# Kernel optimization log

Hardware: AMD Instinct MI355X
Metric: run time of the kernel (lower is better)

Reference implementation:

```python
import jax, jax.numpy as jnp
import numpy as np
import math

N_NODES = 4096
DEG = 32
N_EDGES = N_NODES * DEG
H = 128
NUM_NODE_STATES = 4
NUM_EDGE_STATES = 4
NUM_GRAPHS = 64
UPPER_T, LOWER_T, NUM_ITERS, TEMP_EVAL = 1.0, 0.1, 10000, 0.1
TRAINING_STEP = 1000
NEG_INF = -1.0e9


def temp_by_step(step):
    # linear anneal upper->lower over NUM_ITERS; eval temp when step == -1
    if step == -1:
        return TEMP_EVAL
    frac = min(step / float(NUM_ITERS), 1.0)
    return UPPER_T + (LOWER_T - UPPER_T) * frac


def from_binary_states(bits):
    w = 2 ** jnp.arange(bits.shape[-1], dtype=jnp.int32)
    return jnp.sum(bits.astype(jnp.int32) * w, axis=-1)


def group_argmax_onehot(vals, group, num_segments):
    # gumbel_softmax(vals, group, tau=0, use_noise=False): one-hot argmax per group
    seg_max = jax.ops.segment_max(vals, group, num_segments=num_segments)
    return (vals >= seg_max[group]).astype(jnp.int32)


def layernorm(x, g, b, eps=1e-5):
    mu = jnp.mean(x, -1, keepdims=True)
    var = jnp.mean((x - mu) ** 2, -1, keepdims=True)
    return (x - mu) * jax.lax.rsqrt(var + eps) * g + b


def select_best(emb, bits, scalars, index, num_index):
    states = 2 * from_binary_states(bits)                  # even state codes
    group = states * num_index + index.astype(jnp.int32)   # unique (state, index) id
    best = group_argmax_onehot(-scalars[:, 0], group, emb.shape[0] * num_index)
    return emb[states + best]


def _forward(node_states, edge_states, scalars, edge_index, batch_vec,
             reverse_idx, edge_pos, training_step,
             emb_virtual, emb_reciever, emb_edge, emb_static,
             w_q, w_k, w_v, w_ek, w_ev, w_comb,
             ln_q_g, ln_q_b, ln_k_g, ln_k_b,
             tg_w1, tg_b1, tg_w2, tg_b2):
    src, dst = edge_index[0], edge_index[1]
    N = node_states.shape[0]
    E = src.shape[0]
    D = E // N  # uniform in-degree (incl. self loop)
    h = w_q.shape[0]

    # per-node scalars come from the self-loop edges (exactly one per node)
    loop_vals = jnp.where((src == dst)[:, None], scalars, 0.0)
    node_scalars = jax.ops.segment_sum(loop_vals, dst, num_segments=N)  # [N,1]

    node_fts = select_best(emb_virtual, node_states, node_scalars, batch_vec, NUM_GRAPHS)
    edge_fts = emb_edge[from_binary_states(edge_states)]

    Q = layernorm(node_fts @ w_q.T, ln_q_g, ln_q_b)
    K = layernorm(node_fts @ w_k.T, ln_k_g, ln_k_b)
    V = node_fts @ w_v.T

    # combined edge K/V
    sb = select_best(emb_reciever, node_states[src], scalars, dst, N)
    sender_s = node_scalars[src]
    reciever_s = node_scalars[dst]
    rlx = (scalars < reciever_s).astype(jnp.int32)
    rlx_d = ((sender_s + scalars) < reciever_s).astype(jnp.int32)
    static_fts = emb_static[(rlx + 2 * rlx_d)[:, 0]]
    combined = jnp.concatenate([edge_fts, edge_fts[reverse_idx], static_fts], axis=-1) @ w_comb.T
    edge_K = sb @ w_ek.T
    edge_V = combined @ w_ev.T

    # dense ragged batch per destination node (to_dense_batch equivalent)
    Kc = K[src] + edge_K
    Vc = V[src] + edge_V
    dense_K = jnp.zeros((N, D, h), Kc.dtype).at[dst, edge_pos].set(Kc)
    dense_V = jnp.zeros((N, D, h), Vc.dtype).at[dst, edge_pos].set(Vc)
    mask = jnp.zeros((N, D), bool).at[dst, edge_pos].set(True)

    logits = jnp.einsum('nh,ndh->nd', Q, dense_K) / math.sqrt(h)
    logits = jnp.where(mask, logits, NEG_INF)
    thr = jax.nn.relu(node_fts @ tg_w1.T + tg_b1) @ tg_w2.T + tg_b2  # [N,1]

    tau = temp_by_step(training_step)
    diff = logits - thr
    soft_mask = jax.nn.sigmoid(diff / tau)
    if training_step == -1:
        sel = (diff >= 0).astype(logits.dtype)
    else:
        beta = min(max(tau, 0.01), 1.0)
        sm = jnp.where(mask, jax.nn.softmax(logits, axis=-1), 0.0)
        hard = (diff >= 0).astype(logits.dtype)
        proxy = (1.0 - beta) * soft_mask + beta * sm
        sel = jax.lax.stop_gradient(hard - proxy) + proxy  # straight-through
    sel = sel * mask.astype(logits.dtype)

    msg = jnp.einsum('nd,ndh->nh', sel, dense_V)  # sum aggregation (attention='hard')
    node_out = node_fts + msg
    edge_out = edge_fts + msg[dst]
    return node_out, edge_out


def _build_graph():
    # ring graph, uniform degree DEG per destination incl. self loop;
    # offsets symmetric so every edge has a reverse edge; dst-sorted.
    offs = [0]
    for k in range(1, DEG // 2):
        offs += [k, -k]
    offs.append(N_NODES // 2)  # self-reverse offset
    offs = np.asarray(offs)
    offs_mod = offs % N_NODES
    rev_t = np.array([int(np.where(offs_mod == ((-o) % N_NODES))[0][0]) for o in offs])
    t = np.tile(np.arange(DEG), N_NODES)
    dst = np.repeat(np.arange(N_NODES), DEG)
    src = (dst + offs[t]) % N_NODES
    reverse_idx = src * DEG + rev_t[t]
    return src, dst, reverse_idx, t


def setup_inputs():
    key = jax.random.key(0)
    ks = jax.random.split(key, 20)
    src, dst, reverse_idx, pos = _build_graph()
    s = 1.0 / math.sqrt(H)
    return {
        "node_states": jax.random.randint(ks[0], (N_NODES, NUM_NODE_STATES), 0, 2, dtype=jnp.int32),
        "edge_states": jax.random.randint(ks[1], (N_EDGES, NUM_EDGE_STATES), 0, 2, dtype=jnp.int32),
        "scalars": jax.random.normal(ks[2], (N_EDGES, 1), jnp.float32),
        "edge_index": jnp.asarray(np.stack([src, dst]), dtype=jnp.int32),
        "batch_vec": jnp.asarray(np.arange(N_NODES) // (N_NODES // NUM_GRAPHS), dtype=jnp.int32),
        "reverse_idx": jnp.asarray(reverse_idx, dtype=jnp.int32),
        "edge_pos": jnp.asarray(pos, dtype=jnp.int32),
        "training_step": TRAINING_STEP,
        "emb_virtual": 0.05 * jax.random.normal(ks[3], (2 ** (NUM_NODE_STATES + 1), H), jnp.float32),
        "emb_reciever": 0.05 * jax.random.normal(ks[4], (2 ** (NUM_NODE_STATES + 1), H), jnp.float32),
        "emb_edge": 0.05 * jax.random.normal(ks[5], (2 ** NUM_EDGE_STATES, H), jnp.float32),
        "emb_static": 0.05 * jax.random.normal(ks[6], (4, H), jnp.float32),
        "w_q": s * jax.random.normal(ks[7], (H, H), jnp.float32),
        "w_k": s * jax.random.normal(ks[8], (H, H), jnp.float32),
        "w_v": s * jax.random.normal(ks[9], (H, H), jnp.float32),
        "w_ek": s * jax.random.normal(ks[10], (H, H), jnp.float32),
        "w_ev": s * jax.random.normal(ks[11], (H, H), jnp.float32),
        "w_comb": s * jax.random.normal(ks[12], (H, 3 * H), jnp.float32),
        "ln_q_g": jnp.ones((H,), jnp.float32),
        "ln_q_b": jnp.zeros((H,), jnp.float32),
        "ln_k_g": jnp.ones((H,), jnp.float32),
        "ln_k_b": jnp.zeros((H,), jnp.float32),
        "tg_w1": s * jax.random.normal(ks[13], (H, H), jnp.float32),
        "tg_b1": jnp.zeros((H,), jnp.float32),
        "tg_w2": s * jax.random.normal(ks[14], (1, H), jnp.float32),
        "tg_b2": jnp.full((1,), -5.0, jnp.float32),
    }


def reference(node_states, edge_states, scalars, edge_index, batch_vec,
              reverse_idx, edge_pos, training_step,
              emb_virtual, emb_reciever, emb_edge, emb_static,
              w_q, w_k, w_v, w_ek, w_ev, w_comb,
              ln_q_g, ln_q_b, ln_k_g, ln_k_b,
              tg_w1, tg_b1, tg_w2, tg_b2):
    return _forward(node_states, edge_states, scalars, edge_index, batch_vec,
                    reverse_idx, edge_pos, training_step,
                    emb_virtual, emb_reciever, emb_edge, emb_static,
                    w_q, w_k, w_v, w_ek, w_ev, w_comb,
                    ln_q_g, ln_q_b, ln_k_g, ln_k_b,
                    tg_w1, tg_b1, tg_w2, tg_b2)
```

## Files before the change

### kernel.cpp

```cpp
#include <hip/hip_runtime.h>

#define N_NODES 4096
#define DEG 32
#define N_EDGES (N_NODES * DEG)
#define H 128
#define NUM_GRAPHS 64

#define WS_NODE_SCALARS 0
#define WS_SEG_NODE     4096
#define WS_SEG_EDGE     6144
#define WS_SINT         137216
#define WS_ES           141312
#define WS_QEMB         272384
#define WS_KEMB         276480
#define WS_VEMB         280576
#define WS_EK           284672
#define WS_C1           288768
#define WS_C2           290816
#define WS_C3           292864
#define WS_EV1          293376
#define WS_EV2          295424
#define WS_EV3          297472
#define WS_QK           297984
#define WS_QEK          299008
#define WS_THR          300032
#define WS_MEMSET_U32   137216

__device__ __forceinline__ unsigned int fkey(float x) {
    unsigned int u = __float_as_uint(x);
    return (u & 0x80000000u) ? ~u : (u | 0x80000000u);
}
__device__ __forceinline__ float funkey(unsigned int k) {
    unsigned int u = (k & 0x80000000u) ? (k & 0x7FFFFFFFu) : ~k;
    return __uint_as_float(u);
}
__device__ __forceinline__ int frombin4(const int* __restrict__ p) {
    return p[0] + (p[1] << 1) + (p[2] << 2) + (p[3] << 3);
}
__device__ __forceinline__ float dot128(const float* __restrict__ a, const float* __restrict__ b) {
    float s = 0.f;
#pragma unroll
    for (int k = 0; k < 128; k += 4) {
        float4 av = *(const float4*)(a + k);
        float4 bv = *(const float4*)(b + k);
        s += av.x * bv.x + av.y * bv.y + av.z * bv.z + av.w * bv.w;
    }
    return s;
}

__device__ __forceinline__ float ln128(float v, int t, const float* __restrict__ g,
                                       const float* __restrict__ bb, float* red) {
    red[t] = v;
    __syncthreads();
    for (int off = 64; off > 0; off >>= 1) {
        if (t < off) red[t] += red[t + off];
        __syncthreads();
    }
    float mu = red[0] / 128.f;
    __syncthreads();
    float c = v - mu;
    red[t] = c * c;
    __syncthreads();
    for (int off = 64; off > 0; off >>= 1) {
        if (t < off) red[t] += red[t + off];
        __syncthreads();
    }
    float var = red[0] / 128.f;
    return c * rsqrtf(var + 1e-5f) * g[t] + bb[t];
}

__global__ __launch_bounds__(128) void k12_precompute_edgescan(
    const int* __restrict__ node_states, const int* __restrict__ edge_states,
    const float* __restrict__ scalars, const int* __restrict__ src,
    const int* __restrict__ dst,
    const float* __restrict__ emb_virtual, const float* __restrict__ emb_reciever,
    const float* __restrict__ emb_edge, const float* __restrict__ emb_static,
    const float* __restrict__ w_q, const float* __restrict__ w_k,
    const float* __restrict__ w_v, const float* __restrict__ w_ek,
    const float* __restrict__ w_comb,
    const float* __restrict__ ln_q_g, const float* __restrict__ ln_q_b,
    const float* __restrict__ ln_k_g, const float* __restrict__ ln_k_b,
    const float* __restrict__ tg_w1, const float* __restrict__ tg_b1,
    const float* __restrict__ tg_w2, const float* __restrict__ tg_b2,
    float* __restrict__ ws) {
    __shared__ float red[128];
    int b = blockIdx.x, t = threadIdx.x;
    unsigned int* wsu = (unsigned int*)ws;
    if (b < 32) {
        float v = dot128(emb_virtual + b * H, w_q + t * H);
        ws[WS_QEMB + b * H + t] = ln128(v, t, ln_q_g, ln_q_b, red);
    } else if (b < 64) {
        int s = b - 32;
        float v = dot128(emb_virtual + s * H, w_k + t * H);
        ws[WS_KEMB + s * H + t] = ln128(v, t, ln_k_g, ln_k_b, red);
    } else if (b < 96) {
        int s = b - 64;
        ws[WS_VEMB + s * H + t] = dot128(emb_virtual + s * H, w_v + t * H);
    } else if (b < 128) {
        int s = b - 96;
        ws[WS_EK + s * H + t] = dot128(emb_reciever + s * H, w_ek + t * H);
    } else if (b < 160) {
        int s = b - 128;
        float hval = fmaxf(dot128(emb_virtual + s * H, tg_w1 + t * H) + tg_b1[t], 0.f);
        red[t] = hval * tg_w2[t];
        __syncthreads();
        for (int off = 64; off > 0; off >>= 1) {
            if (t < off) red[t] += red[t + off];
            __syncthreads();
        }
        if (t == 0) ws[WS_THR + s] = red[0] + tg_b2[0];
    } else if (b < 176) {
        int r = b - 160;
        ws[WS_C1 + r * H + t] = dot128(emb_edge + r * H, w_comb + t * 384);
    } else if (b < 192) {
        int r = b - 176;
        ws[WS_C2 + r * H + t] = dot128(emb_edge + r * H, w_comb + t * 384 + 128);
    } else if (b < 196) {
        int r = b - 192;
        ws[WS_C3 + r * H + t] = dot128(emb_static + r * H, w_comb + t * 384 + 256);
    } else {
        int e = (b - 196) * 128 + t;
        wsu[WS_ES + e] = (unsigned)frombin4(edge_states + e * 4);
        int s = src[e], d0 = dst[e];
        float sc = scalars[e];
        int ss = frombin4(node_states + s * 4);
        atomicMax(&wsu[WS_SEG_EDGE + (2 * ss) * N_NODES + d0], fkey(-sc));
        if (s == d0) atomicAdd(&ws[WS_NODE_SCALARS + d0], sc);
        if (e < N_NODES) wsu[WS_SINT + e] = (unsigned)frombin4(node_states + e * 4);
    }
}

__global__ __launch_bounds__(128) void k3_precompute2(
    const float* __restrict__ w_ev, const int* __restrict__ batch_vec,
    float* __restrict__ ws) {
    int b = blockIdx.x, t = threadIdx.x;
    unsigned int* wsu = (unsigned int*)ws;
    if (b < 16) {
        ws[WS_EV1 + b * H + t] = dot128(ws + WS_C1 + b * H, w_ev + t * H);
    } else if (b < 32) {
        int r = b - 16;
        ws[WS_EV2 + r * H + t] = dot128(ws + WS_C2 + r * H, w_ev + t * H);
    } else if (b < 36) {
        int r = b - 32;
        ws[WS_EV3 + r * H + t] = dot128(ws + WS_C3 + r * H, w_ev + t * H);
    } else if (b < 68) {
        int r = b - 36;
        if (t < 32) {
            ws[WS_QK + r * 32 + t] = dot128(ws + WS_QEMB + r * H, ws + WS_KEMB + t * H);
        } else if (t >= 64 && t < 96) {
            int c = t - 64;
            ws[WS_QEK + r * 32 + c] = dot128(ws + WS_QEMB + r * H, ws + WS_EK + c * H);
        }
    } else {
        int n = (b - 68) * 128 + t;
        if (n < N_NODES) {
            int si = (int)wsu[WS_SINT + n];
            atomicMax(&wsu[WS_SEG_NODE + 2 * si * NUM_GRAPHS + batch_vec[n]],
                      fkey(-ws[WS_NODE_SCALARS + n]));
        }
    }
}

__global__ __launch_bounds__(1024) void k5_node_attn(
    const int* __restrict__ src, const int* __restrict__ batch_vec,
    const int* __restrict__ reverse_idx, const float* __restrict__ scalars,
    const int* __restrict__ training_step, const float* __restrict__ emb_virtual,
    const float* __restrict__ emb_edge, const float* __restrict__ ws,
    float* __restrict__ node_out, float* __restrict__ edge_out) {
    __shared__ float tab_v[32 * H];
    __shared__ float tab_e1[16 * H];
    __shared__ float tab_e2[16 * H];
    __shared__ float tab_e3[4 * H];
    __shared__ float tab_emb[16 * H];
    __shared__ float msg_sh[8 * H];
    __shared__ float sel_sh[256];
    __shared__ unsigned v_sh[256];
    __shared__ int q_sh[8];

    const unsigned int* wsu = (const unsigned int*)ws;
    int tid = threadIdx.x;
    int blk = blockIdx.x;

    for (int i = tid; i < 4096; i += 1024) tab_v[i] = ws[WS_VEMB + i];
    for (int i = tid; i < 2048; i += 1024) tab_e1[i] = ws[WS_EV1 + i];
    for (int i = tid; i < 2048; i += 1024) tab_e2[i] = ws[WS_EV2 + i];
    if (tid < 512) tab_e3[tid] = ws[WS_EV3 + tid];
    for (int i = tid; i < 2048; i += 1024) tab_emb[i] = emb_edge[i];

    if (tid < 256) {
        int ln = tid >> 5, lane = tid & 31;
        int n = blk * 8 + ln;
        int e = blk * 256 + tid;
        int s = src[e];
        float sc = scalars[e];
        int ss = (int)wsu[WS_SINT + s], sd = (int)wsu[WS_SINT + n];
        float ns_s = ws[WS_NODE_SCALARS + s], ns_d = ws[WS_NODE_SCALARS + n];
        int q = 2 * sd +
                ((-ns_d >= funkey(wsu[WS_SEG_NODE + 2 * sd * NUM_GRAPHS + batch_vec[n]])) ? 1 : 0);
        int a = 2 * ss +
                ((-ns_s >= funkey(wsu[WS_SEG_NODE + 2 * ss * NUM_GRAPHS + batch_vec[s]])) ? 1 : 0);
        int sbi = 2 * ss + ((-sc >= funkey(wsu[WS_SEG_EDGE + 2 * ss * N_NODES + n])) ? 1 : 0);
        int rlx = (sc < ns_d) ? 1 : 0;
        int rlxd = (ns_s + sc < ns_d) ? 1 : 0;
        int st = rlx + 2 * rlxd;
        unsigned es_e = wsu[WS_ES + e];
        unsigned es_r = wsu[WS_ES + reverse_idx[e]];
        float logit =
            (ws[WS_QK + q * 32 + a] + ws[WS_QEK + q * 32 + sbi]) * 0.08838834764831845f;
        float thr = ws[WS_THR + q];

        float mx = logit;
#pragma unroll
        for (int off = 16; off > 0; off >>= 1) mx = fmaxf(mx, __shfl_xor(mx, off, 32));
        float ex = __expf(logit - mx);
        float sum = ex;
#pragma unroll
        for (int off = 16; off > 0; off >>= 1) sum += __shfl_xor(sum, off, 32);
        float sm = ex / sum;
        float diff = logit - thr;
        float hard = (diff >= 0.f) ? 1.f : 0.f;
        int step = training_step[0];
        float sel;
        if (step == -1) {
            sel = hard;
        } else {
            float tau = 1.0f + (0.1f - 1.0f) * fminf((float)step / 10000.0f, 1.0f);
            float beta = fminf(fmaxf(tau, 0.01f), 1.0f);
            float soft = 1.f / (1.f + __expf(-diff / tau));
            float proxy = (1.f - beta) * soft + beta * sm;
            sel = (hard - proxy) + proxy;
        }
        sel_sh[tid] = sel;
        v_sh[tid] = (unsigned)a | (es_e << 5) | (es_r << 9) | ((unsigned)st << 13);
        if (lane == 0) q_sh[ln] = q;
    }
    __syncthreads();

    {
        int ln = tid >> 7, t = tid & 127;
        float msg = 0.f;
#pragma unroll 8
        for (int s2 = 0; s2 < 32; ++s2) {
            unsigned v = v_sh[ln * 32 + s2];
            float w = sel_sh[ln * 32 + s2];
            msg += w * (tab_v[(v & 31) * H + t] + tab_e1[((v >> 5) & 15) * H + t] +
                        tab_e2[((v >> 9) & 15) * H + t] + tab_e3[((v >> 13) & 3) * H + t]);
        }
        msg_sh[ln * H + t] = msg;
        int n = blk * 8 + ln;
        node_out[n * H + t] = emb_virtual[q_sh[ln] * H + t] + msg;
    }
    __syncthreads();

    {
        const float4* me = (const float4*)msg_sh;
        const float4* te = (const float4*)tab_emb;
        float4* eo = (float4*)edge_out;
#pragma unroll
        for (int it = 0; it < 8; ++it) {
            int f4 = tid + it * 1024;
            int flat = f4 << 2;
            int ln = flat >> 12;
            int s2 = (flat >> 7) & 31;
            int t0 = flat & 127;
            unsigned v = v_sh[ln * 32 + s2];
            int b4 = (v >> 5) & 15;
            float4 m = me[(ln * H + t0) >> 2];
            float4 em = te[(b4 * H + t0) >> 2];
            float4 r;
            r.x = em.x + m.x;
            r.y = em.y + m.y;
            r.z = em.z + m.z;
            r.w = em.w + m.w;
            eo[(size_t)(blk * 256 + ln * 32 + s2) * 32 + (t0 >> 2)] = r;
        }
    }
}

extern "C" void kernel_launch(void* const* d_in, const int* in_sizes, int n_in,
                              void* d_out, int out_size, void* d_ws, size_t ws_size,
                              hipStream_t stream) {
    (void)in_sizes; (void)n_in; (void)out_size; (void)ws_size;
    const int* node_states = (const int*)d_in[0];
    const int* edge_states = (const int*)d_in[1];
    const float* scalars = (const float*)d_in[2];
    const int* edge_index = (const int*)d_in[3];
    const int* batch_vec = (const int*)d_in[4];
    const int* reverse_idx = (const int*)d_in[5];
    const int* edge_pos = (const int*)d_in[6];
    (void)edge_pos;
    const int* training_step = (const int*)d_in[7];
    const float* emb_virtual = (const float*)d_in[8];
    const float* emb_reciever = (const float*)d_in[9];
    const float* emb_edge = (const float*)d_in[10];
    const float* emb_static = (const float*)d_in[11];
    const float* w_q = (const float*)d_in[12];
    const float* w_k = (const float*)d_in[13];
    const float* w_v = (const float*)d_in[14];
    const float* w_ek = (const float*)d_in[15];
    const float* w_ev = (const float*)d_in[16];
    const float* w_comb = (const float*)d_in[17];
    const float* ln_q_g = (const float*)d_in[18];
    const float* ln_q_b = (const float*)d_in[19];
    const float* ln_k_g = (const float*)d_in[20];
    const float* ln_k_b = (const float*)d_in[21];
    const float* tg_w1 = (const float*)d_in[22];
    const float* tg_b1 = (const float*)d_in[23];
    const float* tg_w2 = (const float*)d_in[24];
    const float* tg_b2 = (const float*)d_in[25];

    float* ws = (float*)d_ws;
    float* node_out = (float*)d_out;
    float* edge_out = node_out + (size_t)N_NODES * H;
    const int* src = edge_index;
    const int* dst = edge_index + N_EDGES;

    hipMemsetAsync(d_ws, 0, (size_t)WS_MEMSET_U32 * 4, stream);
    k12_precompute_edgescan<<<196 + N_EDGES / 128, 128, 0, stream>>>(
        node_states, edge_states, scalars, src, dst, emb_virtual, emb_reciever, emb_edge,
        emb_static, w_q, w_k, w_v, w_ek, w_comb, ln_q_g, ln_q_b, ln_k_g, ln_k_b, tg_w1,
        tg_b1, tg_w2, tg_b2, ws);
    k3_precompute2<<<100, 128, 0, stream>>>(w_ev, batch_vec, ws);
    k5_node_attn<<<N_NODES / 8, 1024, 0, stream>>>(src, batch_vec, reverse_idx, scalars,
                                                   training_step, emb_virtual, emb_edge,
                                                   ws, node_out, edge_out);
}
```

Before: 158.2 us.

## Drop global edge-segment atomics and memset, compute per-destination maxima in shared memory

Result: no change. 155.9 us (-1.5%).

```diff
diff --git a/kernel.cpp b/kernel.cpp
--- a/kernel.cpp
+++ b/kernel.cpp
@@ -8,23 +8,21 @@
 
 #define WS_NODE_SCALARS 0
 #define WS_SEG_NODE     4096
-#define WS_SEG_EDGE     6144
-#define WS_SINT         137216
-#define WS_ES           141312
-#define WS_QEMB         272384
-#define WS_KEMB         276480
-#define WS_VEMB         280576
-#define WS_EK           284672
-#define WS_C1           288768
-#define WS_C2           290816
-#define WS_C3           292864
-#define WS_EV1          293376
-#define WS_EV2          295424
-#define WS_EV3          297472
-#define WS_QK           297984
-#define WS_QEK          299008
-#define WS_THR          300032
-#define WS_MEMSET_U32   137216
+#define WS_SINT         6144
+#define WS_ES           10240
+#define WS_QEMB         141312
+#define WS_KEMB         145408
+#define WS_VEMB         149504
+#define WS_EK           153600
+#define WS_C1           157696
+#define WS_C2           159744
+#define WS_C3           161792
+#define WS_EV1          162304
+#define WS_EV2          164352
+#define WS_EV3          166400
+#define WS_QK           166912
+#define WS_QEK          167936
+#define WS_THR          168960
 
 __device__ __forceinline__ unsigned int fkey(float x) {
     unsigned int u = __float_as_uint(x);
@@ -35,7 +33,8 @@
     return __uint_as_float(u);
 }
 __device__ __forceinline__ int frombin4(const int* __restrict__ p) {
-    return p[0] + (p[1] << 1) + (p[2] << 2) + (p[3] << 3);
+    int4 q = *(const int4*)p;
+    return q.x + (q.y << 1) + (q.z << 2) + (q.w << 3);
 }
 __device__ __forceinline__ float dot128(const float* __restrict__ a, const float* __restrict__ b) {
     float s = 0.f;
@@ -48,28 +47,29 @@
     return s;
 }
 
-__device__ __forceinline__ float ln128(float v, int t, const float* __restrict__ g,
+__device__ __forceinline__ float ln256(float v, int t, const float* __restrict__ g,
                                        const float* __restrict__ bb, float* red) {
+    int h = t & 127;
     red[t] = v;
     __syncthreads();
     for (int off = 64; off > 0; off >>= 1) {
-        if (t < off) red[t] += red[t + off];
-        __syncthreads();
-    }
-    float mu = red[0] / 128.f;
+        if (h < off) red[t] += red[t + off];
+        __syncthreads();
+    }
+    float mu = red[t & 128] / 128.f;
     __syncthreads();
     float c = v - mu;
     red[t] = c * c;
     __syncthreads();
     for (int off = 64; off > 0; off >>= 1) {
-        if (t < off) red[t] += red[t + off];
-        __syncthreads();
-    }
-    float var = red[0] / 128.f;
-    return c * rsqrtf(var + 1e-5f) * g[t] + bb[t];
-}
-
-__global__ __launch_bounds__(128) void k12_precompute_edgescan(
+        if (h < off) red[t] += red[t + off];
+        __syncthreads();
+    }
+    float var = red[t & 128] / 128.f;
+    return c * rsqrtf(var + 1e-5f) * g[h] + bb[h];
+}
+
+__global__ __launch_bounds__(256) void kA(
     const int* __restrict__ node_states, const int* __restrict__ edge_states,
     const float* __restrict__ scalars, const int* __restrict__ src,
     const int* __restrict__ dst,
@@ -83,85 +83,99 @@
     const float* __restrict__ tg_w1, const float* __restrict__ tg_b1,
     const float* __restrict__ tg_w2, const float* __restrict__ tg_b2,
     float* __restrict__ ws) {
-    __shared__ float red[128];
+    __shared__ float red[256];
     int b = blockIdx.x, t = threadIdx.x;
     unsigned int* wsu = (unsigned int*)ws;
-    if (b < 32) {
-        float v = dot128(emb_virtual + b * H, w_q + t * H);
-        ws[WS_QEMB + b * H + t] = ln128(v, t, ln_q_g, ln_q_b, red);
-    } else if (b < 64) {
-        int s = b - 32;
-        float v = dot128(emb_virtual + s * H, w_k + t * H);
-        ws[WS_KEMB + s * H + t] = ln128(v, t, ln_k_g, ln_k_b, red);
-    } else if (b < 96) {
-        int s = b - 64;
-        ws[WS_VEMB + s * H + t] = dot128(emb_virtual + s * H, w_v + t * H);
-    } else if (b < 128) {
-        int s = b - 96;
-        ws[WS_EK + s * H + t] = dot128(emb_reciever + s * H, w_ek + t * H);
-    } else if (b < 160) {
-        int s = b - 128;
-        float hval = fmaxf(dot128(emb_virtual + s * H, tg_w1 + t * H) + tg_b1[t], 0.f);
-        red[t] = hval * tg_w2[t];
-        __syncthreads();
-        for (int off = 64; off > 0; off >>= 1) {
-            if (t < off) red[t] += red[t + off];
+    if (b < 98) {
+        int j = 2 * b + (t >> 7), tt = t & 127;
+        if (j < 32) {
+            float v = dot128(emb_virtual + j * H, w_q + tt * H);
+            ws[WS_QEMB + j * H + tt] = ln256(v, t, ln_q_g, ln_q_b, red);
+        } else if (j < 64) {
+            int s = j - 32;
+            float v = dot128(emb_virtual + s * H, w_k + tt * H);
+            ws[WS_KEMB + s * H + tt] = ln256(v, t, ln_k_g, ln_k_b, red);
+        } else if (j < 96) {
+            int s = j - 64;
+            ws[WS_VEMB + s * H + tt] = dot128(emb_virtual + s * H, w_v + tt * H);
+        } else if (j < 128) {
+            int s = j - 96;
+            ws[WS_EK + s * H + tt] = dot128(emb_reciever + s * H, w_ek + tt * H);
+        } else if (j < 160) {
+            int s = j - 128;
+            float hval = fmaxf(dot128(emb_virtual + s * H, tg_w1 + tt * H) + tg_b1[tt], 0.f);
+            red[t] = hval * tg_w2[tt];
             __syncthreads();
-        }
-        if (t == 0) ws[WS_THR + s] = red[0] + tg_b2[0];
-    } else if (b < 176) {
-        int r = b - 160;
-        ws[WS_C1 + r * H + t] = dot128(emb_edge + r * H, w_comb + t * 384);
-    } else if (b < 192) {
-        int r = b - 176;
-        ws[WS_C2 + r * H + t] = dot128(emb_edge + r * H, w_comb + t * 384 + 128);
-    } else if (b < 196) {
-        int r = b - 192;
-        ws[WS_C3 + r * H + t] = dot128(emb_static + r * H, w_comb + t * 384 + 256);
+            for (int off = 64; off > 0; off >>= 1) {
+                if (tt < off) red[t] += red[t + off];
+                __syncthreads();
+            }
+            if (tt == 0) ws[WS_THR + s] = red[t & 128] + tg_b2[0];
+        } else if (j < 176) {
+            int r = j - 160;
+            ws[WS_C1 + r * H + tt] = dot128(emb_edge + r * H, w_comb + tt * 384);
+        } else if (j < 192) {
+            int r = j - 176;
+            ws[WS_C2 + r * H + tt] = dot128(emb_edge + r * H, w_comb + tt * 384 + 128);
+        } else if (j < 196) {
+            int r = j - 192;
+            ws[WS_C3 + r * H + tt] = dot128(emb_static + r * H, w_comb + tt * 384 + 256);
+        }
+    } else if (b < 114) {
+        __shared__ unsigned arr[64];
+        int b2 = b - 98;
+        int n = b2 * 256 + t;
+        int si = frombin4(node_states + n * 4);
+        wsu[WS_SINT + n] = (unsigned)si;
+        float nsum = 0.f;
+#pragma unroll 8
+        for (int k = 0; k < DEG; ++k) {
+            int e = n * DEG + k;
+            if (src[e] == dst[e]) nsum += scalars[e];
+        }
+        ws[WS_NODE_SCALARS + n] = nsum;
+        if (t < 64) arr[t] = 0u;
+        __syncthreads();
+        atomicMax(&arr[(t >> 6) * 16 + si], fkey(-nsum));
+        __syncthreads();
+        if (t < 64) {
+            int gl = t >> 4, ssi = t & 15;
+            wsu[WS_SEG_NODE + 2 * ssi * NUM_GRAPHS + (b2 * 4 + gl)] = arr[gl * 16 + ssi];
+        }
     } else {
-        int e = (b - 196) * 128 + t;
-        wsu[WS_ES + e] = (unsigned)frombin4(edge_states + e * 4);
-        int s = src[e], d0 = dst[e];
-        float sc = scalars[e];
-        int ss = frombin4(node_states + s * 4);
-        atomicMax(&wsu[WS_SEG_EDGE + (2 * ss) * N_NODES + d0], fkey(-sc));
-        if (s == d0) atomicAdd(&ws[WS_NODE_SCALARS + d0], sc);
-        if (e < N_NODES) wsu[WS_SINT + e] = (unsigned)frombin4(node_states + e * 4);
-    }
-}
-
-__global__ __launch_bounds__(128) void k3_precompute2(
-    const float* __restrict__ w_ev, const int* __restrict__ batch_vec,
-    float* __restrict__ ws) {
+        int base = (b - 114) * 2048;
+#pragma unroll
+        for (int it = 0; it < 8; ++it) {
+            int e = base + it * 256 + t;
+            wsu[WS_ES + e] = (unsigned)frombin4(edge_states + e * 4);
+        }
+    }
+}
+
+__global__ __launch_bounds__(256) void kB(const float* __restrict__ w_ev,
+                                          float* __restrict__ ws) {
     int b = blockIdx.x, t = threadIdx.x;
-    unsigned int* wsu = (unsigned int*)ws;
-    if (b < 16) {
-        ws[WS_EV1 + b * H + t] = dot128(ws + WS_C1 + b * H, w_ev + t * H);
-    } else if (b < 32) {
-        int r = b - 16;
-        ws[WS_EV2 + r * H + t] = dot128(ws + WS_C2 + r * H, w_ev + t * H);
-    } else if (b < 36) {
-        int r = b - 32;
-        ws[WS_EV3 + r * H + t] = dot128(ws + WS_C3 + r * H, w_ev + t * H);
-    } else if (b < 68) {
-        int r = b - 36;
-        if (t < 32) {
-            ws[WS_QK + r * 32 + t] = dot128(ws + WS_QEMB + r * H, ws + WS_KEMB + t * H);
-        } else if (t >= 64 && t < 96) {
-            int c = t - 64;
+    int j = 2 * b + (t >> 7), tt = t & 127;
+    if (j < 16) {
+        ws[WS_EV1 + j * H + tt] = dot128(ws + WS_C1 + j * H, w_ev + tt * H);
+    } else if (j < 32) {
+        int r = j - 16;
+        ws[WS_EV2 + r * H + tt] = dot128(ws + WS_C2 + r * H, w_ev + tt * H);
+    } else if (j < 36) {
+        int r = j - 32;
+        ws[WS_EV3 + r * H + tt] = dot128(ws + WS_C3 + r * H, w_ev + tt * H);
+    } else {
+        int r = j - 36;
+        if (tt < 32) {
+            ws[WS_QK + r * 32 + tt] = dot128(ws + WS_QEMB + r * H, ws + WS_KEMB + tt * H);
+        } else if (tt >= 64 && tt < 96) {
+            int c = tt - 64;
             ws[WS_QEK + r * 32 + c] = dot128(ws + WS_QEMB + r * H, ws + WS_EK + c * H);
         }
-    } else {
-        int n = (b - 68) * 128 + t;
-        if (n < N_NODES) {
-            int si = (int)wsu[WS_SINT + n];
-            atomicMax(&wsu[WS_SEG_NODE + 2 * si * NUM_GRAPHS + batch_vec[n]],
-                      fkey(-ws[WS_NODE_SCALARS + n]));
-        }
-    }
-}
-
-__global__ __launch_bounds__(1024) void k5_node_attn(
+    }
+}
+
+__global__ __launch_bounds__(256) void kC(
     const int* __restrict__ src, const int* __restrict__ batch_vec,
     const int* __restrict__ reverse_idx, const float* __restrict__ scalars,
     const int* __restrict__ training_step, const float* __restrict__ emb_virtual,
@@ -172,43 +186,56 @@
     __shared__ float tab_e2[16 * H];
     __shared__ float tab_e3[4 * H];
     __shared__ float tab_emb[16 * H];
+    __shared__ float tab_qk[1024];
+    __shared__ float tab_qek[1024];
+    __shared__ float tab_thr[32];
     __shared__ float msg_sh[8 * H];
     __shared__ float sel_sh[256];
     __shared__ unsigned v_sh[256];
+    __shared__ unsigned sb16[128];
     __shared__ int q_sh[8];
 
     const unsigned int* wsu = (const unsigned int*)ws;
-    int tid = threadIdx.x;
-    int blk = blockIdx.x;
-
-    for (int i = tid; i < 4096; i += 1024) tab_v[i] = ws[WS_VEMB + i];
-    for (int i = tid; i < 2048; i += 1024) tab_e1[i] = ws[WS_EV1 + i];
-    for (int i = tid; i < 2048; i += 1024) tab_e2[i] = ws[WS_EV2 + i];
-    if (tid < 512) tab_e3[tid] = ws[WS_EV3 + tid];
-    for (int i = tid; i < 2048; i += 1024) tab_emb[i] = emb_edge[i];
-
-    if (tid < 256) {
-        int ln = tid >> 5, lane = tid & 31;
-        int n = blk * 8 + ln;
-        int e = blk * 256 + tid;
+    int tid = threadIdx.x, blk = blockIdx.x;
+
+    for (int i = tid; i < 4096; i += 256) tab_v[i] = ws[WS_VEMB + i];
+    for (int i = tid; i < 2048; i += 256) {
+        tab_e1[i] = ws[WS_EV1 + i];
+        tab_e2[i] = ws[WS_EV2 + i];
+        tab_emb[i] = emb_edge[i];
+    }
+    for (int i = tid; i < 512; i += 256) tab_e3[i] = ws[WS_EV3 + i];
+    for (int i = tid; i < 1024; i += 256) {
+        tab_qk[i] = ws[WS_QK + i];
+        tab_qek[i] = ws[WS_QEK + i];
+    }
+    if (tid < 32) tab_thr[tid] = ws[WS_THR + tid];
+    if (tid < 128) sb16[tid] = 0u;
+    __syncthreads();
+
+    int g = tid >> 5, lane = tid & 31;
+    int n = blk * 8 + g;
+    int e = blk * 256 + tid;
+    {
         int s = src[e];
         float sc = scalars[e];
         int ss = (int)wsu[WS_SINT + s], sd = (int)wsu[WS_SINT + n];
         float ns_s = ws[WS_NODE_SCALARS + s], ns_d = ws[WS_NODE_SCALARS + n];
+        atomicMax(&sb16[g * 16 + ss], fkey(-sc));
         int q = 2 * sd +
                 ((-ns_d >= funkey(wsu[WS_SEG_NODE + 2 * sd * NUM_GRAPHS + batch_vec[n]])) ? 1 : 0);
         int a = 2 * ss +
                 ((-ns_s >= funkey(wsu[WS_SEG_NODE + 2 * ss * NUM_GRAPHS + batch_vec[s]])) ? 1 : 0);
-        int sbi = 2 * ss + ((-sc >= funkey(wsu[WS_SEG_EDGE + 2 * ss * N_NODES + n])) ? 1 : 0);
         int rlx = (sc < ns_d) ? 1 : 0;
         int rlxd = (ns_s + sc < ns_d) ? 1 : 0;
         int st = rlx + 2 * rlxd;
         unsigned es_e = wsu[WS_ES + e];
         unsigned es_r = wsu[WS_ES + reverse_idx[e]];
+        __syncthreads();
+        int sbi = 2 * ss + ((-sc >= funkey(sb16[g * 16 + ss])) ? 1 : 0);
         float logit =
-            (ws[WS_QK + q * 32 + a] + ws[WS_QEK + q * 32 + sbi]) * 0.08838834764831845f;
-        float thr = ws[WS_THR + q];
-
+            (tab_qk[q * 32 + a] + tab_qek[q * 32 + sbi]) * 0.08838834764831845f;
+        float thr = tab_thr[q];
         float mx = logit;
 #pragma unroll
         for (int off = 16; off > 0; off >>= 1) mx = fmaxf(mx, __shfl_xor(mx, off, 32));
@@ -232,23 +259,34 @@
         }
         sel_sh[tid] = sel;
         v_sh[tid] = (unsigned)a | (es_e << 5) | (es_r << 9) | ((unsigned)st << 13);
-        if (lane == 0) q_sh[ln] = q;
+        if (lane == 0) q_sh[g] = q;
     }
     __syncthreads();
 
     {
-        int ln = tid >> 7, t = tid & 127;
-        float msg = 0.f;
+        float4 msg = make_float4(0.f, 0.f, 0.f, 0.f);
+        int vb = g * 32;
 #pragma unroll 8
         for (int s2 = 0; s2 < 32; ++s2) {
-            unsigned v = v_sh[ln * 32 + s2];
-            float w = sel_sh[ln * 32 + s2];
-            msg += w * (tab_v[(v & 31) * H + t] + tab_e1[((v >> 5) & 15) * H + t] +
-                        tab_e2[((v >> 9) & 15) * H + t] + tab_e3[((v >> 13) & 3) * H + t]);
-        }
-        msg_sh[ln * H + t] = msg;
-        int n = blk * 8 + ln;
-        node_out[n * H + t] = emb_virtual[q_sh[ln] * H + t] + msg;
+            unsigned v = v_sh[vb + s2];
+            float w = sel_sh[vb + s2];
+            float4 rv = ((const float4*)(tab_v + (v & 31) * H))[lane];
+            float4 r1 = ((const float4*)(tab_e1 + ((v >> 5) & 15) * H))[lane];
+            float4 r2 = ((const float4*)(tab_e2 + ((v >> 9) & 15) * H))[lane];
+            float4 r3 = ((const float4*)(tab_e3 + ((v >> 13) & 3) * H))[lane];
+            msg.x += w * (rv.x + r1.x + r2.x + r3.x);
+            msg.y += w * (rv.y + r1.y + r2.y + r3.y);
+            msg.z += w * (rv.z + r1.z + r2.z + r3.z);
+            msg.w += w * (rv.w + r1.w + r2.w + r3.w);
+        }
+        ((float4*)msg_sh)[tid] = msg;
+        float4 ev = ((const float4*)(emb_virtual + q_sh[g] * H))[lane];
+        float4 r;
+        r.x = ev.x + msg.x;
+        r.y = ev.y + msg.y;
+        r.z = ev.z + msg.z;
+        r.w = ev.w + msg.w;
+        ((float4*)node_out)[n * 32 + lane] = r;
     }
     __syncthreads();
 
@@ -256,23 +294,21 @@
         const float4* me = (const float4*)msg_sh;
         const float4* te = (const float4*)tab_emb;
         float4* eo = (float4*)edge_out;
-#pragma unroll
-        for (int it = 0; it < 8; ++it) {
-            int f4 = tid + it * 1024;
-            int flat = f4 << 2;
-            int ln = flat >> 12;
-            int s2 = (flat >> 7) & 31;
-            int t0 = flat & 127;
-            unsigned v = v_sh[ln * 32 + s2];
+        size_t base = (size_t)blk * 8192;
+#pragma unroll
+        for (int it = 0; it < 32; ++it) {
+            int idx = it * 256 + tid;
+            int ed = idx >> 5, p = idx & 31;
+            unsigned v = v_sh[ed];
             int b4 = (v >> 5) & 15;
-            float4 m = me[(ln * H + t0) >> 2];
-            float4 em = te[(b4 * H + t0) >> 2];
+            float4 m = me[(ed >> 5) * 32 + p];
+            float4 em = te[b4 * 32 + p];
             float4 r;
             r.x = em.x + m.x;
             r.y = em.y + m.y;
             r.z = em.z + m.z;
             r.w = em.w + m.w;
-            eo[(size_t)(blk * 256 + ln * 32 + s2) * 32 + (t0 >> 2)] = r;
+            eo[base + idx] = r;
         }
     }
 }
@@ -287,8 +323,6 @@
     const int* edge_index = (const int*)d_in[3];
     const int* batch_vec = (const int*)d_in[4];
     const int* reverse_idx = (const int*)d_in[5];
-    const int* edge_pos = (const int*)d_in[6];
-    (void)edge_pos;
     const int* training_step = (const int*)d_in[7];
     const float* emb_virtual = (const float*)d_in[8];
     const float* emb_reciever = (const float*)d_in[9];
@@ -315,13 +349,12 @@
     const int* src = edge_index;
     const int* dst = edge_index + N_EDGES;
 
-    hipMemsetAsync(d_ws, 0, (size_t)WS_MEMSET_U32 * 4, stream);
-    k12_precompute_edgescan<<<196 + N_EDGES / 128, 128, 0, stream>>>(
-        node_states, edge_states, scalars, src, dst, emb_virtual, emb_reciever, emb_edge,
-        emb_static, w_q, w_k, w_v, w_ek, w_comb, ln_q_g, ln_q_b, ln_k_g, ln_k_b, tg_w1,
-        tg_b1, tg_w2, tg_b2, ws);
-    k3_precompute2<<<100, 128, 0, stream>>>(w_ev, batch_vec, ws);
-    k5_node_attn<<<N_NODES / 8, 1024, 0, stream>>>(src, batch_vec, reverse_idx, scalars,
-                                                   training_step, emb_virtual, emb_edge,
-                                                   ws, node_out, edge_out);
-}
+    kA<<<178, 256, 0, stream>>>(node_states, edge_states, scalars, src, dst, emb_virtual,
+                                emb_reciever, emb_edge, emb_static, w_q, w_k, w_v, w_ek,
+                                w_comb, ln_q_g, ln_q_b, ln_k_g, ln_k_b, tg_w1, tg_b1,
+                                tg_w2, tg_b2, ws);
+    kB<<<34, 256, 0, stream>>>(w_ev, ws);
+    kC<<<N_NODES / 8, 256, 0, stream>>>(src, batch_vec, reverse_idx, scalars,
+                                        training_step, emb_virtual, emb_edge, ws,
+                                        node_out, edge_out);
+}
```
